# Optimization experiments

Measured on AMD Instinct MI355X. Metric: run time of the kernel, lower is better.

## Reference

```python
import jax, jax.numpy as jnp
import numpy as np

D_MODEL = 1024
N_HEADS = 16
HEAD_DIM = 64
D_FF = 4096


def rmsnorm(x, w):
    eps = jnp.finfo(x.dtype).eps
    var = jnp.mean(jnp.square(x), axis=-1, keepdims=True)
    return x * jax.lax.rsqrt(var + eps) * w


def setup_inputs() -> dict:
    key = jax.random.key(0)
    ks = jax.random.split(key, 8)
    d, h, hd, dff = D_MODEL, N_HEADS, HEAD_DIM, D_FF
    s = 0.02
    return {
        "x": jax.random.normal(ks[0], (2, 2048, d), dtype=jnp.float32),
        "norm_w": jnp.ones((d,), dtype=jnp.float32),
        "Wq": jax.random.normal(ks[1], (d, h * hd), dtype=jnp.float32) * s,
        "Wk": jax.random.normal(ks[2], (d, h * hd), dtype=jnp.float32) * s,
        "Wv": jax.random.normal(ks[3], (d, h * hd), dtype=jnp.float32) * s,
        "Wo": jax.random.normal(ks[4], (h * hd, d), dtype=jnp.float32) * s,
        "W1": jax.random.normal(ks[5], (d, dff), dtype=jnp.float32) * s,
        "W2": jax.random.normal(ks[6], (dff, d), dtype=jnp.float32) * s,
    }


def reference(x, norm_w, Wq, Wk, Wv, Wo, W1, W2):
    B, T, d = x.shape
    h, hd = N_HEADS, HEAD_DIM
    scale = 1.0 / np.sqrt(hd)

    xn = rmsnorm(x, norm_w)

    # attention branch
    q = (xn @ Wq).reshape(B, T, h, hd).transpose(0, 2, 1, 3)  # [B,h,T,hd]
    k = (xn @ Wk).reshape(B, T, h, hd).transpose(0, 2, 1, 3)
    v = (xn @ Wv).reshape(B, T, h, hd).transpose(0, 2, 1, 3)
    attn = jnp.einsum("bhqd,bhkd->bhqk", q, k) * scale
    causal = jnp.tril(jnp.ones((T, T), dtype=bool))
    attn = jnp.where(causal, attn, -jnp.inf)
    attn = jax.nn.softmax(attn, axis=-1)
    out = jnp.einsum("bhqk,bhkd->bhqd", attn, v)
    out = out.transpose(0, 2, 1, 3).reshape(B, T, h * hd)
    attn_out = out @ Wo

    # FFN branch
    ffn_out = jax.nn.silu(xn @ W1) @ W2

    return x + attn_out + ffn_out
```

## Files before the change

kernel.cpp:

```cpp
#include <hip/hip_runtime.h>

#define DM   1024
#define DFF  4096
#define NH   16
#define HD   64
#define TT   2048
#define BT   4096

typedef unsigned short u16;
typedef unsigned int   u32;
typedef __attribute__((ext_vector_type(8))) short s16x8;
typedef __attribute__((ext_vector_type(4))) float f32x4;

__device__ __forceinline__ u16 f2bf(float f) {
  u32 u = __builtin_bit_cast(u32, f);
  u += 0x7fffu + ((u >> 16) & 1u);
  return (u16)(u >> 16);
}

__device__ __forceinline__ void gl2lds16(const void* g, void* l) {
  __builtin_amdgcn_global_load_lds((__attribute__((address_space(1))) void*)(g),
                                   (__attribute__((address_space(3))) void*)(l),
                                   16, 0, 0);
}

__global__ __launch_bounds__(256) void rmsnorm_k(const float* __restrict__ x,
                                                 const float* __restrict__ w,
                                                 u16* __restrict__ xn,
                                                 float* __restrict__ dout) {
  const int row = blockIdx.x;
  const int t = threadIdx.x;
  const float4 v = ((const float4*)(x + (size_t)row * DM))[t];
  ((float4*)(dout + (size_t)row * DM))[t] = v;
  float ss = v.x*v.x + v.y*v.y + v.z*v.z + v.w*v.w;
  #pragma unroll
  for (int off = 32; off; off >>= 1) ss += __shfl_xor(ss, off, 64);
  __shared__ float red[4];
  if ((t & 63) == 0) red[t >> 6] = ss;
  __syncthreads();
  const float tot = red[0] + red[1] + red[2] + red[3];
  const float r = __builtin_amdgcn_rsqf(tot * (1.0f / DM) + 1.1920929e-7f);
  const float4 wv = ((const float4*)w)[t];
  u16* o = xn + (size_t)row * DM + t * 4;
  o[0] = f2bf(v.x * r * wv.x);
  o[1] = f2bf(v.y * r * wv.y);
  o[2] = f2bf(v.z * r * wv.z);
  o[3] = f2bf(v.w * r * wv.w);
}

__global__ __launch_bounds__(256) void wtrans_k(const float* __restrict__ W,
                                                u16* __restrict__ Wt,
                                                int K, int N) {
  __shared__ float tile[32][33];
  const int n0 = blockIdx.x * 32, k0 = blockIdx.y * 32;
  const int tx = threadIdx.x, ty = threadIdx.y;
  #pragma unroll
  for (int i = 0; i < 4; ++i)
    tile[ty + i*8][tx] = W[(size_t)(k0 + ty + i*8) * N + n0 + tx];
  __syncthreads();
  #pragma unroll
  for (int i = 0; i < 4; ++i)
    Wt[(size_t)(n0 + ty + i*8) * K + k0 + tx] = f2bf(tile[tx][ty + i*8]);
}

__global__ __launch_bounds__(256, 2) void gemm_fused(const u16* __restrict__ A,
                                                     const u16* __restrict__ Bt,
                                                     u16* __restrict__ qkb,
                                                     u16* __restrict__ vtg,
                                                     u16* __restrict__ ff1) {
  const int K = 1024;
  __shared__ u16 sA[128 * 32];
  __shared__ u16 sB[128 * 32];
  const int t = threadIdx.x;
  const int lane = t & 63, wave = t >> 6;
  const int quad = lane >> 4, l4 = lane & 15;
  const int wy = wave >> 1, wx = wave & 1;
  const size_t mBase = (size_t)blockIdx.y * 128;
  const size_t nBase = (size_t)blockIdx.x * 128;
  const int r  = t >> 2;
  const int c8 = (t & 3) * 8;
  const u16* Ag0 = A + (mBase + r) * K + c8;
  const u16* Ag1 = Ag0 + (size_t)64 * K;
  const u16* Bg0 = Bt + (nBase + r) * K + c8;
  const u16* Bg1 = Bg0 + (size_t)64 * K;
  char* sAb = (char*)sA + (wave << 10);
  char* sBb = (char*)sB + (wave << 10);

  f32x4 acc[4][4];
  #pragma unroll
  for (int i = 0; i < 4; ++i)
    #pragma unroll
    for (int j = 0; j < 4; ++j)
      acc[i][j] = (f32x4)0.0f;

  for (int k0 = 0; k0 < K; k0 += 32) {
    __syncthreads();
    gl2lds16(Ag0 + k0, sAb);
    gl2lds16(Ag1 + k0, sAb + 4096);
    gl2lds16(Bg0 + k0, sBb);
    gl2lds16(Bg1 + k0, sBb + 4096);
    __syncthreads();
    s16x8 af[4], bfr[4];
    #pragma unroll
    for (int i = 0; i < 4; ++i)
      af[i] = *(const s16x8*)&sA[(wy*64 + i*16 + l4) * 32 + quad*8];
    #pragma unroll
    for (int j = 0; j < 4; ++j)
      bfr[j] = *(const s16x8*)&sB[(wx*64 + j*16 + l4) * 32 + quad*8];
    #pragma unroll
    for (int i = 0; i < 4; ++i)
      #pragma unroll
      for (int j = 0; j < 4; ++j)
        acc[i][j] = __builtin_amdgcn_mfma_f32_16x16x32_bf16(af[i], bfr[j], acc[i][j], 0, 0, 0);
  }

  #pragma unroll
  for (int i = 0; i < 4; ++i) {
    const size_t row0 = mBase + wy*64 + i*16 + quad*4;
    #pragma unroll
    for (int j = 0; j < 4; ++j) {
      const int col = (int)nBase + wx*64 + j*16 + l4;
      if (nBase < 1024) {
        #pragma unroll
        for (int rg = 0; rg < 4; ++rg)
          qkb[(row0 + rg) * 2048 + col] = f2bf(acc[i][j][rg] * 0.18033688011f);
      } else if (nBase < 2048) {
        #pragma unroll
        for (int rg = 0; rg < 4; ++rg)
          qkb[(row0 + rg) * 2048 + col] = f2bf(acc[i][j][rg]);
      } else if (nBase < 3072) {
        const int cv = col - 2048, hh = cv >> 6, dd = cv & 63;
        const int bb = (int)(row0 >> 11), t0 = (int)(row0 & 2047);
        ushort4 pk;
        pk.x = f2bf(acc[i][j][0]); pk.y = f2bf(acc[i][j][1]);
        pk.z = f2bf(acc[i][j][2]); pk.w = f2bf(acc[i][j][3]);
        *(ushort4*)(vtg + ((size_t)((bb*16 + hh)*64 + dd)) * 2048 + t0) = pk;
      } else {
        #pragma unroll
        for (int rg = 0; rg < 4; ++rg) {
          float v = acc[i][j][rg];
          v = v / (1.0f + __expf(-v));
          ff1[(row0 + rg) * (size_t)DFF + (col - 3072)] = f2bf(v);
        }
      }
    }
  }
}

__global__ __launch_bounds__(256, 2) void gemm_atomic(const u16* __restrict__ A,
                                                      const u16* __restrict__ Bt,
                                                      float* __restrict__ out,
                                                      int K, int KS) {
  const int N = 1024;
  __shared__ u16 sA[128 * 32];
  __shared__ u16 sB[128 * 32];
  const int t = threadIdx.x;
  const int lane = t & 63, wave = t >> 6;
  const int quad = lane >> 4, l4 = lane & 15;
  const int wy = wave >> 1, wx = wave & 1;
  const size_t mBase = (size_t)blockIdx.y * 128;
  const size_t nBase = (size_t)blockIdx.x * 128;
  const int kBase = blockIdx.z * KS;
  const int r  = t >> 2;
  const int c8 = (t & 3) * 8;
  const u16* Ag0 = A + (mBase + r) * K + kBase + c8;
  const u16* Ag1 = Ag0 + (size_t)64 * K;
  const u16* Bg0 = Bt + (nBase + r) * K + kBase + c8;
  const u16* Bg1 = Bg0 + (size_t)64 * K;
  char* sAb = (char*)sA + (wave << 10);
  char* sBb = (char*)sB + (wave << 10);

  f32x4 acc[4][4];
  #pragma unroll
  for (int i = 0; i < 4; ++i)
    #pragma unroll
    for (int j = 0; j < 4; ++j)
      acc[i][j] = (f32x4)0.0f;

  for (int k0 = 0; k0 < KS; k0 += 32) {
    __syncthreads();
    gl2lds16(Ag0 + k0, sAb);
    gl2lds16(Ag1 + k0, sAb + 4096);
    gl2lds16(Bg0 + k0, sBb);
    gl2lds16(Bg1 + k0, sBb + 4096);
    __syncthreads();
    s16x8 af[4], bfr[4];
    #pragma unroll
    for (int i = 0; i < 4; ++i)
      af[i] = *(const s16x8*)&sA[(wy*64 + i*16 + l4) * 32 + quad*8];
    #pragma unroll
    for (int j = 0; j < 4; ++j)
      bfr[j] = *(const s16x8*)&sB[(wx*64 + j*16 + l4) * 32 + quad*8];
    #pragma unroll
    for (int i = 0; i < 4; ++i)
      #pragma unroll
      for (int j = 0; j < 4; ++j)
        acc[i][j] = __builtin_amdgcn_mfma_f32_16x16x32_bf16(af[i], bfr[j], acc[i][j], 0, 0, 0);
  }

  #pragma unroll
  for (int i = 0; i < 4; ++i) {
    const size_t row0 = mBase + wy*64 + i*16 + quad*4;
    #pragma unroll
    for (int j = 0; j < 4; ++j) {
      const int col = (int)nBase + wx*64 + j*16 + l4;
      #pragma unroll
      for (int rg = 0; rg < 4; ++rg)
        unsafeAtomicAdd(&out[(row0 + rg) * (size_t)N + col], acc[i][j][rg]);
    }
  }
}

__global__ __launch_bounds__(128) void attn_k(const u16* __restrict__ qk,
                                              const u16* __restrict__ vtg,
                                              u16* __restrict__ ao) {
  const int bh = blockIdx.x, b = bh >> 4, h = bh & 15;
  const int qt = 63 - blockIdx.y;
  const int qw = qt * 32;
  const int wave = threadIdx.x >> 6, lane = threadIdx.x & 63;
  const int quad = lane >> 4, l4 = lane & 15;
  const u16* Qp = qk + (size_t)b * TT * 2048 + h * HD;
  const u16* Kp = Qp + 1024;
  const u16* Vp = vtg + (size_t)bh * 64 * 2048;

  __shared__ u16 Pb[2][32][72];
  __shared__ float Ob[32][68];
  __shared__ float Lb[32];

  s16x8 qf[2][2];
  #pragma unroll
  for (int mi = 0; mi < 2; ++mi)
    #pragma unroll
    for (int kf = 0; kf < 2; ++kf)
      qf[mi][kf] = *(const s16x8*)(Qp + (size_t)(qw + mi*16 + l4) * 2048 + kf*32 + quad*8);

  const s16x8 ones = {0x3F80,0x3F80,0x3F80,0x3F80,0x3F80,0x3F80,0x3F80,0x3F80};

  f32x4 o[2][4];
  f32x4 lacc[2];
  #pragma unroll
  for (int mi = 0; mi < 2; ++mi) {
    lacc[mi] = (f32x4)0.0f;
    #pragma unroll
    for (int ni = 0; ni < 4; ++ni) o[mi][ni] = (f32x4)0.0f;
  }

  const int n   = (qt + 2) >> 1;
  const int n0  = (n + 1) >> 1;
  const int kt0 = wave ? n0 : 0;
  const int kt1 = wave ? n : n0;

  for (int kt = kt0; kt < kt1; ++kt) {
    const int k0 = kt * 64;

    f32x4 st[4][2];
    #pragma unroll
    for (int nj = 0; nj < 4; ++nj) {
      const u16* kr = Kp + (size_t)(k0 + nj*16 + l4) * 2048 + quad*8;
      const s16x8 kf0 = *(const s16x8*)kr;
      const s16x8 kf1 = *(const s16x8*)(kr + 32);
      #pragma unroll
      for (int mi = 0; mi < 2; ++mi) {
        f32x4 a = (f32x4)0.0f;
        a = __builtin_amdgcn_mfma_f32_16x16x32_bf16(kf0, qf[mi][0], a, 0, 0, 0);
        a = __builtin_amdgcn_mfma_f32_16x16x32_bf16(kf1, qf[mi][1], a, 0, 0, 0);
        st[nj][mi] = a;
      }
    }

    s16x8 vb[2][4];
    #pragma unroll
    for (int kf2 = 0; kf2 < 2; ++kf2)
      #pragma unroll
      for (int ni = 0; ni < 4; ++ni)
        vb[kf2][ni] = *(const s16x8*)(Vp + (size_t)(ni*16 + l4) * 2048 + k0 + kf2*32 + quad*8);

    if (k0 + 63 > qw) {
      #pragma unroll
      for (int nj = 0; nj < 4; ++nj)
        #pragma unroll
        for (int mi = 0; mi < 2; ++mi)
          #pragma unroll
          for (int rg = 0; rg < 4; ++rg) {
            const int key = k0 + nj*16 + quad*4 + rg;
            const int q   = qw + mi*16 + l4;
            if (key > q) st[nj][mi][rg] = -1e30f;
          }
    }

    #pragma unroll
    for (int nj = 0; nj < 4; ++nj)
      #pragma unroll
      for (int mi = 0; mi < 2; ++mi) {
        float p0 = __builtin_amdgcn_exp2f(st[nj][mi][0]);
        float p1 = __builtin_amdgcn_exp2f(st[nj][mi][1]);
        float p2 = __builtin_amdgcn_exp2f(st[nj][mi][2]);
        float p3 = __builtin_amdgcn_exp2f(st[nj][mi][3]);
        uint2 w;
        w.x = __builtin_amdgcn_perm(__builtin_bit_cast(u32, p1),
                                    __builtin_bit_cast(u32, p0), 0x07060302u);
        w.y = __builtin_amdgcn_perm(__builtin_bit_cast(u32, p3),
                                    __builtin_bit_cast(u32, p2), 0x07060302u);
        *(uint2*)&Pb[wave][mi*16 + l4][nj*16 + quad*4] = w;
      }

    #pragma unroll
    for (int kf2 = 0; kf2 < 2; ++kf2) {
      s16x8 pa[2];
      #pragma unroll
      for (int mi = 0; mi < 2; ++mi)
        pa[mi] = *(const s16x8*)&Pb[wave][mi*16 + l4][kf2*32 + quad*8];
      #pragma unroll
      for (int mi = 0; mi < 2; ++mi) {
        lacc[mi] = __builtin_amdgcn_mfma_f32_16x16x32_bf16(pa[mi], ones, lacc[mi], 0, 0, 0);
        #pragma unroll
        for (int ni = 0; ni < 4; ++ni)
          o[mi][ni] = __builtin_amdgcn_mfma_f32_16x16x32_bf16(pa[mi], vb[kf2][ni], o[mi][ni], 0, 0, 0);
      }
    }
  }

  if (wave == 1) {
    #pragma unroll
    for (int mi = 0; mi < 2; ++mi)
      #pragma unroll
      for (int rg = 0; rg < 4; ++rg) {
        const int row = mi*16 + quad*4 + rg;
        #pragma unroll
        for (int ni = 0; ni < 4; ++ni) Ob[row][ni*16 + l4] = o[mi][ni][rg];
        if (l4 == 0) Lb[row] = lacc[mi][rg];
      }
  }
  __syncthreads();
  if (wave == 0) {
    #pragma unroll
    for (int mi = 0; mi < 2; ++mi)
      #pragma unroll
      for (int rg = 0; rg < 4; ++rg) {
        const int row = mi*16 + quad*4 + rg;
        const float inv = 1.0f / (lacc[mi][rg] + Lb[row]);
        #pragma unroll
        for (int ni = 0; ni < 4; ++ni)
          Pb[0][row][ni*16 + l4] = f2bf((o[mi][ni][rg] + Ob[row][ni*16 + l4]) * inv);
      }
    #pragma unroll
    for (int it = 0; it < 4; ++it) {
      const int row = it*8 + (lane >> 3);
      const int c0  = (lane & 7) * 8;
      const s16x8 pk = *(const s16x8*)&Pb[0][row][c0];
      *(s16x8*)(ao + ((size_t)b * TT + qw + row) * DM + h*HD + c0) = pk;
    }
  }
}

extern "C" void kernel_launch(void* const* d_in, const int* in_sizes, int n_in,
                              void* d_out, int out_size, void* d_ws, size_t ws_size,
                              hipStream_t stream) {
  (void)in_sizes; (void)n_in; (void)out_size; (void)ws_size;
  const float* x  = (const float*)d_in[0];
  const float* nw = (const float*)d_in[1];
  const float* Wq = (const float*)d_in[2];
  const float* Wk = (const float*)d_in[3];
  const float* Wv = (const float*)d_in[4];
  const float* Wo = (const float*)d_in[5];
  const float* W1 = (const float*)d_in[6];
  const float* W2 = (const float*)d_in[7];

  char* ws = (char*)d_ws;
  u16*   xn      = (u16*)(ws);
  u16*   wqkv1_t = (u16*)(ws + ((size_t)8  << 20));
  u16*   wo_t    = (u16*)(ws + ((size_t)22 << 20));
  u16*   w2_t    = (u16*)(ws + ((size_t)24 << 20));
  u16*   qkb     = (u16*)(ws + ((size_t)32 << 20));
  u16*   vtg     = (u16*)(ws + ((size_t)48 << 20));
  u16*   attn_o  = (u16*)(ws + ((size_t)56 << 20));
  u16*   ff1     = (u16*)(ws + ((size_t)64 << 20));
  float* dout    = (float*)d_out;

  rmsnorm_k<<<BT, 256, 0, stream>>>(x, nw, xn, dout);
  const dim3 tb(32, 8);
  wtrans_k<<<dim3(32, 32),  tb, 0, stream>>>(Wq, wqkv1_t,                      1024, 1024);
  wtrans_k<<<dim3(32, 32),  tb, 0, stream>>>(Wk, wqkv1_t + (size_t)1024*1024,  1024, 1024);
  wtrans_k<<<dim3(32, 32),  tb, 0, stream>>>(Wv, wqkv1_t + (size_t)2048*1024,  1024, 1024);
  wtrans_k<<<dim3(128, 32), tb, 0, stream>>>(W1, wqkv1_t + (size_t)3072*1024,  1024, 4096);
  wtrans_k<<<dim3(32, 32),  tb, 0, stream>>>(Wo, wo_t,                         1024, 1024);
  wtrans_k<<<dim3(32, 128), tb, 0, stream>>>(W2, w2_t,                         4096, 1024);

  gemm_fused<<<dim3(56, 32), 256, 0, stream>>>(xn, wqkv1_t, qkb, vtg, ff1);
  gemm_atomic<<<dim3(8, 32, 2), 256, 0, stream>>>(ff1, w2_t, dout, 4096, 2048);
  attn_k<<<dim3(32, 64), 128, 0, stream>>>(qkb, vtg, attn_o);
  gemm_atomic<<<dim3(8, 32, 2), 256, 0, stream>>>(attn_o, wo_t, dout, 1024, 512);
}
```

Measured before the change: 381.8 us.

## Merge Wo and W2 projections into one K-concatenated GEMM with residual epilogue

The attention output and the SiLU FFN activations are now written side by side into one [4096 x 5120] activation buffer. Wo and W2 are transposed into a matching concatenated weight buffer. A single GEMM with K=5120 then writes x + result directly, replacing two split-K atomic GEMMs and the residual copy done in rmsnorm. This removes the fp32 atomic traffic and an extra launch. In exchange the grid drops to 256 blocks of 512 threads with a long, unpipelined K loop, so latency hiding depends on the 8 waves per block.

```diff
diff --git a/kernel.cpp b/kernel.cpp
--- a/kernel.cpp
+++ b/kernel.cpp
@@ -6,6 +6,7 @@
 #define HD   64
 #define TT   2048
 #define BT   4096
+#define KC   5120
 
 typedef unsigned short u16;
 typedef unsigned int   u32;
@@ -26,12 +27,10 @@
 
 __global__ __launch_bounds__(256) void rmsnorm_k(const float* __restrict__ x,
                                                  const float* __restrict__ w,
-                                                 u16* __restrict__ xn,
-                                                 float* __restrict__ dout) {
+                                                 u16* __restrict__ xn) {
   const int row = blockIdx.x;
   const int t = threadIdx.x;
   const float4 v = ((const float4*)(x + (size_t)row * DM))[t];
-  ((float4*)(dout + (size_t)row * DM))[t] = v;
   float ss = v.x*v.x + v.y*v.y + v.z*v.z + v.w*v.w;
   #pragma unroll
   for (int off = 32; off; off >>= 1) ss += __shfl_xor(ss, off, 64);
@@ -50,7 +49,7 @@
 
 __global__ __launch_bounds__(256) void wtrans_k(const float* __restrict__ W,
                                                 u16* __restrict__ Wt,
-                                                int K, int N) {
+                                                int K, int N, int pitch, int koff) {
   __shared__ float tile[32][33];
   const int n0 = blockIdx.x * 32, k0 = blockIdx.y * 32;
   const int tx = threadIdx.x, ty = threadIdx.y;
@@ -60,14 +59,14 @@
   __syncthreads();
   #pragma unroll
   for (int i = 0; i < 4; ++i)
-    Wt[(size_t)(n0 + ty + i*8) * K + k0 + tx] = f2bf(tile[tx][ty + i*8]);
+    Wt[(size_t)(n0 + ty + i*8) * pitch + koff + k0 + tx] = f2bf(tile[tx][ty + i*8]);
 }
 
 __global__ __launch_bounds__(256, 2) void gemm_fused(const u16* __restrict__ A,
                                                      const u16* __restrict__ Bt,
                                                      u16* __restrict__ qkb,
                                                      u16* __restrict__ vtg,
-                                                     u16* __restrict__ ff1) {
+                                                     u16* __restrict__ acat) {
   const int K = 1024;
   __shared__ u16 sA[128 * 32];
   __shared__ u16 sB[128 * 32];
@@ -140,61 +139,55 @@
         for (int rg = 0; rg < 4; ++rg) {
           float v = acc[i][j][rg];
           v = v / (1.0f + __expf(-v));
-          ff1[(row0 + rg) * (size_t)DFF + (col - 3072)] = f2bf(v);
+          acat[(row0 + rg) * (size_t)KC + 1024 + (col - 3072)] = f2bf(v);
         }
       }
     }
   }
 }
 
-__global__ __launch_bounds__(256, 2) void gemm_atomic(const u16* __restrict__ A,
-                                                      const u16* __restrict__ Bt,
-                                                      float* __restrict__ out,
-                                                      int K, int KS) {
-  const int N = 1024;
+__global__ __launch_bounds__(512) void gemm_final(const u16* __restrict__ A,
+                                                  const u16* __restrict__ Bt,
+                                                  const float* __restrict__ x,
+                                                  float* __restrict__ out) {
   __shared__ u16 sA[128 * 32];
   __shared__ u16 sB[128 * 32];
   const int t = threadIdx.x;
   const int lane = t & 63, wave = t >> 6;
   const int quad = lane >> 4, l4 = lane & 15;
-  const int wy = wave >> 1, wx = wave & 1;
+  const int wy = wave >> 2, wx = wave & 3;
   const size_t mBase = (size_t)blockIdx.y * 128;
   const size_t nBase = (size_t)blockIdx.x * 128;
-  const int kBase = blockIdx.z * KS;
   const int r  = t >> 2;
   const int c8 = (t & 3) * 8;
-  const u16* Ag0 = A + (mBase + r) * K + kBase + c8;
-  const u16* Ag1 = Ag0 + (size_t)64 * K;
-  const u16* Bg0 = Bt + (nBase + r) * K + kBase + c8;
-  const u16* Bg1 = Bg0 + (size_t)64 * K;
+  const u16* Ag = A  + (mBase + r) * KC + c8;
+  const u16* Bg = Bt + (nBase + r) * KC + c8;
   char* sAb = (char*)sA + (wave << 10);
   char* sBb = (char*)sB + (wave << 10);
 
-  f32x4 acc[4][4];
+  f32x4 acc[4][2];
   #pragma unroll
   for (int i = 0; i < 4; ++i)
     #pragma unroll
-    for (int j = 0; j < 4; ++j)
+    for (int j = 0; j < 2; ++j)
       acc[i][j] = (f32x4)0.0f;
 
-  for (int k0 = 0; k0 < KS; k0 += 32) {
+  for (int k0 = 0; k0 < KC; k0 += 32) {
     __syncthreads();
-    gl2lds16(Ag0 + k0, sAb);
-    gl2lds16(Ag1 + k0, sAb + 4096);
-    gl2lds16(Bg0 + k0, sBb);
-    gl2lds16(Bg1 + k0, sBb + 4096);
+    gl2lds16(Ag + k0, sAb);
+    gl2lds16(Bg + k0, sBb);
     __syncthreads();
-    s16x8 af[4], bfr[4];
+    s16x8 af[4], bfr[2];
     #pragma unroll
     for (int i = 0; i < 4; ++i)
       af[i] = *(const s16x8*)&sA[(wy*64 + i*16 + l4) * 32 + quad*8];
     #pragma unroll
-    for (int j = 0; j < 4; ++j)
-      bfr[j] = *(const s16x8*)&sB[(wx*64 + j*16 + l4) * 32 + quad*8];
+    for (int j = 0; j < 2; ++j)
+      bfr[j] = *(const s16x8*)&sB[(wx*32 + j*16 + l4) * 32 + quad*8];
     #pragma unroll
     for (int i = 0; i < 4; ++i)
       #pragma unroll
-      for (int j = 0; j < 4; ++j)
+      for (int j = 0; j < 2; ++j)
         acc[i][j] = __builtin_amdgcn_mfma_f32_16x16x32_bf16(af[i], bfr[j], acc[i][j], 0, 0, 0);
   }
 
@@ -202,18 +195,20 @@
   for (int i = 0; i < 4; ++i) {
     const size_t row0 = mBase + wy*64 + i*16 + quad*4;
     #pragma unroll
-    for (int j = 0; j < 4; ++j) {
-      const int col = (int)nBase + wx*64 + j*16 + l4;
-      #pragma unroll
-      for (int rg = 0; rg < 4; ++rg)
-        unsafeAtomicAdd(&out[(row0 + rg) * (size_t)N + col], acc[i][j][rg]);
+    for (int j = 0; j < 2; ++j) {
+      const int col = (int)nBase + wx*32 + j*16 + l4;
+      #pragma unroll
+      for (int rg = 0; rg < 4; ++rg) {
+        const size_t idx = (row0 + rg) * (size_t)DM + col;
+        out[idx] = x[idx] + acc[i][j][rg];
+      }
     }
   }
 }
 
 __global__ __launch_bounds__(128) void attn_k(const u16* __restrict__ qk,
                                               const u16* __restrict__ vtg,
-                                              u16* __restrict__ ao) {
+                                              u16* __restrict__ acat) {
   const int bh = blockIdx.x, b = bh >> 4, h = bh & 15;
   const int qt = 63 - blockIdx.y;
   const int qw = qt * 32;
@@ -348,7 +343,7 @@
       const int row = it*8 + (lane >> 3);
       const int c0  = (lane & 7) * 8;
       const s16x8 pk = *(const s16x8*)&Pb[0][row][c0];
-      *(s16x8*)(ao + ((size_t)b * TT + qw + row) * DM + h*HD + c0) = pk;
+      *(s16x8*)(acat + ((size_t)b * TT + qw + row) * KC + h*HD + c0) = pk;
     }
   }
 }
@@ -369,25 +364,22 @@
   char* ws = (char*)d_ws;
   u16*   xn      = (u16*)(ws);
   u16*   wqkv1_t = (u16*)(ws + ((size_t)8  << 20));
-  u16*   wo_t    = (u16*)(ws + ((size_t)22 << 20));
-  u16*   w2_t    = (u16*)(ws + ((size_t)24 << 20));
+  u16*   bcat    = (u16*)(ws + ((size_t)22 << 20));
   u16*   qkb     = (u16*)(ws + ((size_t)32 << 20));
   u16*   vtg     = (u16*)(ws + ((size_t)48 << 20));
-  u16*   attn_o  = (u16*)(ws + ((size_t)56 << 20));
-  u16*   ff1     = (u16*)(ws + ((size_t)64 << 20));
+  u16*   acat    = (u16*)(ws + ((size_t)56 << 20));
   float* dout    = (float*)d_out;
 
-  rmsnorm_k<<<BT, 256, 0, stream>>>(x, nw, xn, dout);
+  rmsnorm_k<<<BT, 256, 0, stream>>>(x, nw, xn);
   const dim3 tb(32, 8);
-  wtrans_k<<<dim3(32, 32),  tb, 0, stream>>>(Wq, wqkv1_t,                      1024, 1024);
-  wtrans_k<<<dim3(32, 32),  tb, 0, stream>>>(Wk, wqkv1_t + (size_t)1024*1024,  1024, 1024);
-  wtrans_k<<<dim3(32, 32),  tb, 0, stream>>>(Wv, wqkv1_t + (size_t)2048*1024,  1024, 1024);
-  wtrans_k<<<dim3(128, 32), tb, 0, stream>>>(W1, wqkv1_t + (size_t)3072*1024,  1024, 4096);
-  wtrans_k<<<dim3(32, 32),  tb, 0, stream>>>(Wo, wo_t,                         1024, 1024);
-  wtrans_k<<<dim3(32, 128), tb, 0, stream>>>(W2, w2_t,                         4096, 1024);
-
-  gemm_fused<<<dim3(56, 32), 256, 0, stream>>>(xn, wqkv1_t, qkb, vtg, ff1);
-  gemm_atomic<<<dim3(8, 32, 2), 256, 0, stream>>>(ff1, w2_t, dout, 4096, 2048);
-  attn_k<<<dim3(32, 64), 128, 0, stream>>>(qkb, vtg, attn_o);
-  gemm_atomic<<<dim3(8, 32, 2), 256, 0, stream>>>(attn_o, wo_t, dout, 1024, 512);
-}
+  wtrans_k<<<dim3(32, 32),  tb, 0, stream>>>(Wq, wqkv1_t,                      1024, 1024, 1024, 0);
+  wtrans_k<<<dim3(32, 32),  tb, 0, stream>>>(Wk, wqkv1_t + (size_t)1024*1024,  1024, 1024, 1024, 0);
+  wtrans_k<<<dim3(32, 32),  tb, 0, stream>>>(Wv, wqkv1_t + (size_t)2048*1024,  1024, 1024, 1024, 0);
+  wtrans_k<<<dim3(128, 32), tb, 0, stream>>>(W1, wqkv1_t + (size_t)3072*1024,  1024, 4096, 1024, 0);
+  wtrans_k<<<dim3(32, 32),  tb, 0, stream>>>(Wo, bcat,                         1024, 1024, 5120, 0);
+  wtrans_k<<<dim3(32, 128), tb, 0, stream>>>(W2, bcat,                         4096, 1024, 5120, 1024);
+
+  gemm_fused<<<dim3(56, 32), 256, 0, stream>>>(xn, wqkv1_t, qkb, vtg, acat);
+  attn_k<<<dim3(32, 64), 128, 0, stream>>>(qkb, vtg, acat);
+  gemm_final<<<dim3(8, 32), 512, 0, stream>>>(acat, bcat, x, dout);
+}
```

Result: no change. 377.2 us (-1.2%).
